# Optimization experiments

Measured on AMD Instinct MI355X. Metric: run time of the kernel, lower is better.

The kernel has to match this reference:

```python
import jax, jax.numpy as jnp
import numpy as np

N = 100000   # num_nodes
E = 300000   # num directed edges (symmetrized to 2E inside forward)
D = 128      # input_dim
O = 128      # output_dim
R = 32       # num_relations
B = 8        # num_bases


def setup_inputs() -> dict:
    key = jax.random.key(0)
    ks = jax.random.split(key, 8)
    x = jax.random.normal(ks[0], (N, D), dtype=jnp.float32)
    node_keep_mask = jax.random.randint(ks[1], (N,), 0, 2) > 0
    source = jax.random.randint(ks[2], (E,), 0, N, dtype=jnp.int32)
    target = jax.random.randint(ks[3], (E,), 0, N, dtype=jnp.int32)
    edge_type = jax.random.randint(ks[4], (E,), 0, R, dtype=jnp.int32)
    edge_weights = jax.random.uniform(ks[5], (E,), dtype=jnp.float32)
    # xavier_normal for bases
    std = (2.0 / (D + O)) ** 0.5
    bases = jax.random.normal(ks[6], (B, D, O), dtype=jnp.float32) * std
    # uniform then L1-normalized rows, shape (R+1, B); row R is the self-loop
    rbw = jax.random.uniform(ks[7], (R + 1, B), dtype=jnp.float32)
    rbw = rbw / jnp.sum(rbw, axis=1, keepdims=True)
    return {
        "x": x,
        "node_keep_mask": node_keep_mask,
        "source": source,
        "target": target,
        "edge_type": edge_type,
        "edge_weights": edge_weights,
        "bases": bases,
        "relation_base_weights": rbw,
    }


def reference(x, node_keep_mask, source, target, edge_type, edge_weights,
              bases, relation_base_weights):
    # Self-loop: weight for relation id == num_relations (last row)
    w_self = jnp.einsum("bij,b->ij", bases, relation_base_weights[-1])
    out = jnp.where(node_keep_mask[:, None], x @ w_self, jnp.zeros((), x.dtype))

    # Symmetrize edges: messages flow in both directions (same relation/weight)
    src = jnp.concatenate([source, target])          # (2E,)
    tgt = jnp.concatenate([target, source])          # (2E,)
    etype = jnp.concatenate([edge_type, edge_type])  # (2E,)
    ew = jnp.concatenate([edge_weights, edge_weights])  # (2E,)

    # Project all nodes through every basis once: (N, B, O)
    proj = jnp.einsum("nd,bdo->nbo", x, bases)
    # Per-edge basis coefficients from the edge's relation: (2E, B)
    coeff = relation_base_weights[etype]
    # Message: x[src] @ (sum_b coeff_b * base_b) == sum_b coeff_b * proj[src, b]
    msg = jnp.einsum("eb,ebo->eo", coeff, proj[src])  # (2E, O)
    msg = msg * ew[:, None]

    # Scatter-add messages into target nodes
    out = out.at[tgt].add(msg)
    return out
```

## Files before the change

### kernel.cpp

```cpp
#include <hip/hip_runtime.h>

typedef __attribute__((ext_vector_type(8))) __bf16 bf16x8;
typedef __attribute__((ext_vector_type(4))) float f32x4;
typedef __attribute__((ext_vector_type(8))) unsigned short ushortx8;

__device__ inline unsigned short f2bf(float f) {
  unsigned int u = __float_as_uint(f);
  unsigned int r = (u + 0x7FFFu + ((u >> 16) & 1u)) >> 16;
  return (unsigned short)r;
}

__global__ __launch_bounds__(256) void conv_kernel(const float* __restrict__ x,
                                                   unsigned short* __restrict__ xb,
                                                   int total8) {
  int id = blockIdx.x * 256 + threadIdx.x;
  if (id >= total8) return;
  f32x4 f0 = ((const f32x4*)x)[2 * id];
  f32x4 f1 = ((const f32x4*)x)[2 * id + 1];
  ushortx8 r;
  r[0] = f2bf(f0[0]); r[1] = f2bf(f0[1]); r[2] = f2bf(f0[2]); r[3] = f2bf(f0[3]);
  r[4] = f2bf(f1[0]); r[5] = f2bf(f1[1]); r[6] = f2bf(f1[2]); r[7] = f2bf(f1[3]);
  ((ushortx8*)xb)[id] = r;
}

__global__ __launch_bounds__(256) void tconv_kernel(const float* __restrict__ bases,
                                                    unsigned short* __restrict__ bmt) {
  int id = blockIdx.x * 256 + threadIdx.x;
  if (id >= 128 * 1024) return;
  int o = id >> 10, k = id & 1023, b = k >> 7, d = k & 127;
  bmt[id] = f2bf(bases[b * 16384 + d * 128 + o]);
}

__global__ void detect_kernel(const unsigned char* __restrict__ mask, int nbytes,
                              int* __restrict__ flag_out) {
  __shared__ int nz_off, big;
  if (threadIdx.x == 0) { nz_off = 0; big = 0; }
  __syncthreads();
  int lnz = 0, lbig = 0;
  for (int i = threadIdx.x; i < nbytes; i += 256) {
    unsigned char v = mask[i];
    if ((i & 3) && v) lnz++;
    if (v > 1) lbig++;
  }
  if (lnz) atomicAdd(&nz_off, lnz);
  if (lbig) atomicAdd(&big, lbig);
  __syncthreads();
  if (threadIdx.x == 0) *flag_out = (nz_off == 0) ? 0 : ((big == 0) ? 1 : 2);
}

__global__ __launch_bounds__(256) void hist_kernel(const int* __restrict__ src,
                                                   const int* __restrict__ tgt, int E,
                                                   int* __restrict__ cnt) {
  int i = blockIdx.x * 256 + threadIdx.x;
  if (i >= E) return;
  atomicAdd(&cnt[tgt[i]], 1);
  atomicAdd(&cnt[src[i]], 1);
}

__global__ __launch_bounds__(256) void scan1_kernel(const int* __restrict__ cnt, int N,
                                                    int* __restrict__ bsum) {
  __shared__ int s[256];
  int t = threadIdx.x, i = blockIdx.x * 256 + t;
  s[t] = (i < N) ? cnt[i] : 0;
  __syncthreads();
#pragma unroll
  for (int off = 128; off > 0; off >>= 1) {
    if (t < off) s[t] += s[t + off];
    __syncthreads();
  }
  if (t == 0) bsum[blockIdx.x] = s[0];
}

__global__ void scan2_kernel(const int* __restrict__ bsum, int nb,
                             int* __restrict__ bexcl, int* __restrict__ base, int N) {
  __shared__ int s[512];
  int t = threadIdx.x;
  int v = (t < nb) ? bsum[t] : 0;
  s[t] = v;
  __syncthreads();
  for (int off = 1; off < 512; off <<= 1) {
    int x = (t >= off) ? s[t - off] : 0;
    __syncthreads();
    s[t] += x;
    __syncthreads();
  }
  if (t < nb) bexcl[t] = s[t] - v;
  if (t == nb - 1) base[N] = s[t];
}

__global__ __launch_bounds__(256) void scan3_kernel(const int* __restrict__ cnt, int N,
                                                    const int* __restrict__ bexcl,
                                                    int* __restrict__ base,
                                                    int* __restrict__ cursor) {
  __shared__ int s[256];
  int t = threadIdx.x, i = blockIdx.x * 256 + t;
  int c = (i < N) ? cnt[i] : 0;
  s[t] = c;
  __syncthreads();
  for (int off = 1; off < 256; off <<= 1) {
    int x = (t >= off) ? s[t - off] : 0;
    __syncthreads();
    s[t] += x;
    __syncthreads();
  }
  if (i < N) {
    int v = bexcl[blockIdx.x] + s[t] - c;
    base[i] = v;
    cursor[i] = v;
  }
}

__global__ __launch_bounds__(256) void scatter_kernel(const int* __restrict__ src,
                                                      const int* __restrict__ tgt,
                                                      const int* __restrict__ et,
                                                      const float* __restrict__ ew, int E,
                                                      int* __restrict__ cursor,
                                                      uint2* __restrict__ msrw) {
  int i = blockIdx.x * 256 + threadIdx.x;
  if (i >= E) return;
  int s = src[i], g = tgt[i], r = et[i];
  unsigned wbits = __float_as_uint(ew[i]);
  int s1 = atomicAdd(&cursor[g], 1);
  msrw[s1] = make_uint2((unsigned)s | ((unsigned)r << 24), wbits);
  int s2 = atomicAdd(&cursor[s], 1);
  msrw[s2] = make_uint2((unsigned)g | ((unsigned)r << 24), wbits);
}

__global__ __launch_bounds__(512, 4) void gather_kernel(
    const unsigned* __restrict__ xb32, const unsigned short* __restrict__ bmt,
    const int* __restrict__ base, const uint2* __restrict__ msrw,
    const float* __restrict__ rbw, const void* __restrict__ maskp,
    const int* __restrict__ flag_p, float* __restrict__ out, int N) {
  extern __shared__ char smem[];
  float* ctab = (float*)(smem + 65536);
  int t = threadIdx.x;
  for (int i = t; i < 264; i += 512) ctab[i] = rbw[i];
  int wid = t >> 6, l = t & 63;
  int t0 = blockIdx.x * 32;
  int flag = *flag_p;
  __syncthreads();

#pragma unroll
  for (int pr = 0; pr < 2; ++pr) {
    int tgA = t0 + wid * 4 + pr * 2;
    int tgc[2], beg[2], cnt[2];
    float zlo[2][8], zhi[2][8];
    uint2 srw0[2], srw1[2];
    unsigned x0[2];
#pragma unroll
    for (int p = 0; p < 2; ++p) {
      int tg = tgA + p;
      tgc[p] = (tg < N) ? tg : (N - 1);
    }
    int b0 = base[tgc[0]], b1 = base[tgc[0] + 1], b2 = base[tgc[1] + 1];
    beg[0] = b0; cnt[0] = (tgA < N) ? (b1 - b0) : 0;
    beg[1] = base[tgc[1]];
    cnt[1] = (tgA + 1 < N) ? (b2 - beg[1]) : 0;
#pragma unroll
    for (int p = 0; p < 2; ++p) {
      int tg = tgA + p;
      unsigned xs = xb32[(size_t)tgc[p] * 64 + l];
      bool keep;
      if (flag == 0)      keep = ((const int*)maskp)[tgc[p]] != 0;
      else if (flag == 1) keep = ((const unsigned char*)maskp)[tgc[p]] != 0;
      else                keep = ((const float*)maskp)[tgc[p]] != 0.f;
      float ms = (keep && tg < N) ? 1.f : 0.f;
      float slo = __uint_as_float(xs << 16);
      float shi = __uint_as_float(xs & 0xFFFF0000u);
#pragma unroll
      for (int b = 0; b < 8; ++b) {
        float a = ms * ctab[256 + b];
        zlo[p][b] = a * slo;
        zhi[p][b] = a * shi;
      }
      srw0[p] = make_uint2(0u, 0u);
      srw1[p] = make_uint2(0u, 0u);
      x0[p] = 0u;
      if (cnt[p] > 0) srw0[p] = msrw[beg[p]];
      if (cnt[p] > 1) srw1[p] = msrw[beg[p] + 1];
      if (cnt[p] > 0) x0[p] = xb32[(size_t)(srw0[p].x & 0xFFFFFFu) * 64 + l];
    }
    int mmax = max(cnt[0], cnt[1]);
    for (int m = 0; m < mmax; ++m) {
#pragma unroll
      for (int p = 0; p < 2; ++p) {
        if (m < cnt[p]) {
          int i2 = (m + 2 < cnt[p]) ? (beg[p] + m + 2) : beg[p];
          uint2 srw2 = msrw[i2];
          unsigned x1 = xb32[(size_t)(srw1[p].x & 0xFFFFFFu) * 64 + l];
          int rel = srw0[p].x >> 24;
          float w = __uint_as_float(srw0[p].y);
          f32x4 c0 = *(const f32x4*)&ctab[rel * 8];
          f32x4 c1 = *(const f32x4*)&ctab[rel * 8 + 4];
          float cc[8] = {c0[0], c0[1], c0[2], c0[3], c1[0], c1[1], c1[2], c1[3]};
          float lo = __uint_as_float(x0[p] << 16);
          float hi = __uint_as_float(x0[p] & 0xFFFF0000u);
#pragma unroll
          for (int b = 0; b < 8; ++b) {
            float a = w * cc[b];
            zlo[p][b] = fmaf(a, lo, zlo[p][b]);
            zhi[p][b] = fmaf(a, hi, zhi[p][b]);
          }
          srw0[p] = srw1[p]; x0[p] = x1; srw1[p] = srw2;
        }
      }
    }
#pragma unroll
    for (int p = 0; p < 2; ++p) {
      int row = wid * 4 + pr * 2 + p;
#pragma unroll
      for (int b = 0; b < 8; ++b) {
        unsigned pk = (unsigned)f2bf(zlo[p][b]) | ((unsigned)f2bf(zhi[p][b]) << 16);
        int byte = row * 2048 + ((b * 256 + l * 4) ^ ((row & 7) << 4));
        *(unsigned*)(smem + byte) = pk;
      }
    }
  }
  __syncthreads();

  int l15 = l & 15, lk8 = (l >> 4) * 8;
  f32x4 acc[2] = {};
  for (int ks = 0; ks < 32; ++ks) {
    int k0 = ks * 32 + lk8;
    bf16x8 a[2], bb;
#pragma unroll
    for (int rt = 0; rt < 2; ++rt) {
      int tr = rt * 16 + l15;
      int byte = tr * 2048 + ((k0 * 2) ^ ((tr & 7) << 4));
      a[rt] = *(const bf16x8*)(smem + byte);
    }
    int col = wid * 16 + l15;
    bb = *(const bf16x8*)(bmt + (size_t)col * 1024 + k0);
#pragma unroll
    for (int rt = 0; rt < 2; ++rt)
      acc[rt] = __builtin_amdgcn_mfma_f32_16x16x32_bf16(a[rt], bb, acc[rt], 0, 0, 0);
  }
#pragma unroll
  for (int rt = 0; rt < 2; ++rt) {
    int rowb = t0 + rt * 16 + (l >> 4) * 4;
    int col = wid * 16 + l15;
#pragma unroll
    for (int i = 0; i < 4; ++i) {
      int row = rowb + i;
      if (row < N) out[(size_t)row * 128 + col] = acc[rt][i];
    }
  }
}

extern "C" void kernel_launch(void* const* d_in, const int* in_sizes, int n_in,
                              void* d_out, int out_size, void* d_ws, size_t ws_size,
                              hipStream_t stream) {
  const float* x = (const float*)d_in[0];
  const void* mask = d_in[1];
  const int* source = (const int*)d_in[2];
  const int* target = (const int*)d_in[3];
  const int* etype = (const int*)d_in[4];
  const float* eweight = (const float*)d_in[5];
  const float* bases = (const float*)d_in[6];
  const float* rbw = (const float*)d_in[7];
  float* out = (float*)d_out;

  const int N = in_sizes[1];
  const int E = in_sizes[2];
  const int M = 2 * E;
  const int NB = (N + 255) / 256;

  char* ws = (char*)d_ws;
  size_t off = 0;
  unsigned short* xb = (unsigned short*)(ws + off); off += (size_t)N * 256;
  unsigned short* bmt = (unsigned short*)(ws + off); off += 128 * 1024 * 2;
  uint2* msrw = (uint2*)(ws + off); off += (size_t)(M + 4) * 8;
  int* base = (int*)(ws + off); off += ((size_t)N + 64) * 4;
  int* cursor = (int*)(ws + off); off += ((size_t)N + 64) * 4;
  int* cnt = (int*)(ws + off); off += ((size_t)N + 64) * 4;
  int* bsum = (int*)(ws + off); off += 2048;
  int* bexcl = (int*)(ws + off); off += 2048;
  int* flag = (int*)(ws + off); off += 256;

  hipMemsetAsync(cnt, 0, (size_t)N * 4, stream);
  detect_kernel<<<1, 256, 0, stream>>>((const unsigned char*)mask, N < 8192 ? N : 8192, flag);
  int total8 = (N * 128) / 8;
  conv_kernel<<<(total8 + 255) / 256, 256, 0, stream>>>(x, xb, total8);
  tconv_kernel<<<(128 * 1024 + 255) / 256, 256, 0, stream>>>(bases, bmt);
  hist_kernel<<<(E + 255) / 256, 256, 0, stream>>>(source, target, E, cnt);
  scan1_kernel<<<NB, 256, 0, stream>>>(cnt, N, bsum);
  scan2_kernel<<<1, 512, 0, stream>>>(bsum, NB, bexcl, base, N);
  scan3_kernel<<<NB, 256, 0, stream>>>(cnt, N, bexcl, base, cursor);
  scatter_kernel<<<(E + 255) / 256, 256, 0, stream>>>(source, target, etype, eweight, E,
                                                      cursor, msrw);
  int gblk = (N + 31) / 32;
  size_t shmem = 65536 + 264 * sizeof(float) + 16;
  gather_kernel<<<gblk, 512, shmem, stream>>>((const unsigned*)xb, bmt, base, msrw,
                                              rbw, mask, flag, out, N);
}
```

Baseline: 283.0 us.

## Fuse prep kernels and batch edge-metadata loads per warp with shuffles

Merges the bf16 conversion of x, the transposed conversion of bases and the mask-format detection into one launch using block-range dispatch, removing two kernel launches. In the gather kernel, each warp now handles its four target nodes one after another. It loads up to 64 edge records at once (one per lane), broadcasts them with shuffles, and issues eight independent x-row gathers before doing the FMAs. This replaces the serial two-deep prefetch chain, which aims to expose more memory-level parallelism, at the cost of extra shuffles and more register pressure.

Measured after the change: 279.9 us. About the same (-1.1%).

```diff
diff --git a/kernel.cpp b/kernel.cpp
--- a/kernel.cpp
+++ b/kernel.cpp
@@ -10,42 +10,43 @@
   return (unsigned short)r;
 }
 
-__global__ __launch_bounds__(256) void conv_kernel(const float* __restrict__ x,
-                                                   unsigned short* __restrict__ xb,
-                                                   int total8) {
-  int id = blockIdx.x * 256 + threadIdx.x;
-  if (id >= total8) return;
-  f32x4 f0 = ((const f32x4*)x)[2 * id];
-  f32x4 f1 = ((const f32x4*)x)[2 * id + 1];
-  ushortx8 r;
-  r[0] = f2bf(f0[0]); r[1] = f2bf(f0[1]); r[2] = f2bf(f0[2]); r[3] = f2bf(f0[3]);
-  r[4] = f2bf(f1[0]); r[5] = f2bf(f1[1]); r[6] = f2bf(f1[2]); r[7] = f2bf(f1[3]);
-  ((ushortx8*)xb)[id] = r;
-}
-
-__global__ __launch_bounds__(256) void tconv_kernel(const float* __restrict__ bases,
-                                                    unsigned short* __restrict__ bmt) {
-  int id = blockIdx.x * 256 + threadIdx.x;
-  if (id >= 128 * 1024) return;
-  int o = id >> 10, k = id & 1023, b = k >> 7, d = k & 127;
-  bmt[id] = f2bf(bases[b * 16384 + d * 128 + o]);
-}
-
-__global__ void detect_kernel(const unsigned char* __restrict__ mask, int nbytes,
-                              int* __restrict__ flag_out) {
-  __shared__ int nz_off, big;
-  if (threadIdx.x == 0) { nz_off = 0; big = 0; }
-  __syncthreads();
-  int lnz = 0, lbig = 0;
-  for (int i = threadIdx.x; i < nbytes; i += 256) {
-    unsigned char v = mask[i];
-    if ((i & 3) && v) lnz++;
-    if (v > 1) lbig++;
-  }
-  if (lnz) atomicAdd(&nz_off, lnz);
-  if (lbig) atomicAdd(&big, lbig);
-  __syncthreads();
-  if (threadIdx.x == 0) *flag_out = (nz_off == 0) ? 0 : ((big == 0) ? 1 : 2);
+__global__ __launch_bounds__(256) void prep_kernel(const float* __restrict__ x,
+                                                   unsigned short* __restrict__ xb, int total8,
+                                                   const float* __restrict__ bases,
+                                                   unsigned short* __restrict__ bmt,
+                                                   const unsigned char* __restrict__ mask,
+                                                   int mbytes, int* __restrict__ flag_out,
+                                                   int CB, int TB) {
+  int bid = blockIdx.x;
+  if (bid < CB) {
+    int id = bid * 256 + threadIdx.x;
+    if (id >= total8) return;
+    f32x4 f0 = ((const f32x4*)x)[2 * id];
+    f32x4 f1 = ((const f32x4*)x)[2 * id + 1];
+    ushortx8 r;
+    r[0] = f2bf(f0[0]); r[1] = f2bf(f0[1]); r[2] = f2bf(f0[2]); r[3] = f2bf(f0[3]);
+    r[4] = f2bf(f1[0]); r[5] = f2bf(f1[1]); r[6] = f2bf(f1[2]); r[7] = f2bf(f1[3]);
+    ((ushortx8*)xb)[id] = r;
+  } else if (bid < CB + TB) {
+    int id = (bid - CB) * 256 + threadIdx.x;
+    if (id >= 128 * 1024) return;
+    int o = id >> 10, k = id & 1023, b = k >> 7, d = k & 127;
+    bmt[id] = f2bf(bases[b * 16384 + d * 128 + o]);
+  } else {
+    __shared__ int nz_off, big;
+    if (threadIdx.x == 0) { nz_off = 0; big = 0; }
+    __syncthreads();
+    int lnz = 0, lbig = 0;
+    for (int i = threadIdx.x; i < mbytes; i += 256) {
+      unsigned char v = mask[i];
+      if ((i & 3) && v) lnz++;
+      if (v > 1) lbig++;
+    }
+    if (lnz) atomicAdd(&nz_off, lnz);
+    if (lbig) atomicAdd(&big, lbig);
+    __syncthreads();
+    if (threadIdx.x == 0) *flag_out = (nz_off == 0) ? 0 : ((big == 0) ? 1 : 2);
+  }
 }
 
 __global__ __launch_bounds__(256) void hist_kernel(const int* __restrict__ src,
@@ -140,80 +141,95 @@
   int flag = *flag_p;
   __syncthreads();
 
-#pragma unroll
-  for (int pr = 0; pr < 2; ++pr) {
-    int tgA = t0 + wid * 4 + pr * 2;
-    int tgc[2], beg[2], cnt[2];
-    float zlo[2][8], zhi[2][8];
-    uint2 srw0[2], srw1[2];
-    unsigned x0[2];
-#pragma unroll
-    for (int p = 0; p < 2; ++p) {
-      int tg = tgA + p;
-      tgc[p] = (tg < N) ? tg : (N - 1);
-    }
-    int b0 = base[tgc[0]], b1 = base[tgc[0] + 1], b2 = base[tgc[1] + 1];
-    beg[0] = b0; cnt[0] = (tgA < N) ? (b1 - b0) : 0;
-    beg[1] = base[tgc[1]];
-    cnt[1] = (tgA + 1 < N) ? (b2 - beg[1]) : 0;
-#pragma unroll
-    for (int p = 0; p < 2; ++p) {
-      int tg = tgA + p;
-      unsigned xs = xb32[(size_t)tgc[p] * 64 + l];
-      bool keep;
-      if (flag == 0)      keep = ((const int*)maskp)[tgc[p]] != 0;
-      else if (flag == 1) keep = ((const unsigned char*)maskp)[tgc[p]] != 0;
-      else                keep = ((const float*)maskp)[tgc[p]] != 0.f;
-      float ms = (keep && tg < N) ? 1.f : 0.f;
-      float slo = __uint_as_float(xs << 16);
-      float shi = __uint_as_float(xs & 0xFFFF0000u);
+  int tgbase = t0 + wid * 4;
+  int bv = 0;
+  if (l < 5) bv = base[min(tgbase + (int)l, N)];
+  int baseArr[5];
+#pragma unroll
+  for (int j = 0; j < 5; ++j) baseArr[j] = __shfl(bv, j);
+
+  unsigned xself[4];
+  float msk[4];
+#pragma unroll
+  for (int j = 0; j < 4; ++j) {
+    int tg = tgbase + j;
+    int tgc = min(tg, N - 1);
+    xself[j] = xb32[(size_t)tgc * 64 + l];
+    bool keep;
+    if (flag == 0)      keep = ((const int*)maskp)[tgc] != 0;
+    else if (flag == 1) keep = ((const unsigned char*)maskp)[tgc] != 0;
+    else                keep = ((const float*)maskp)[tgc] != 0.f;
+    msk[j] = (keep && tg < N) ? 1.f : 0.f;
+  }
+
+  uint2 srwl = make_uint2(0u, 0u);
+  {
+    int c = (tgbase < N) ? (baseArr[1] - baseArr[0]) : 0;
+    if (c > 0) srwl = msrw[baseArr[0] + min((int)l, c - 1)];
+  }
+
+  for (int j = 0; j < 4; ++j) {
+    int tg = tgbase + j;
+    int beg = baseArr[j];
+    int cnt = (tg < N) ? (baseArr[j + 1] - beg) : 0;
+    float zlo[8], zhi[8];
+    {
+      float slo = __uint_as_float(xself[j] << 16);
+      float shi = __uint_as_float(xself[j] & 0xFFFF0000u);
 #pragma unroll
       for (int b = 0; b < 8; ++b) {
-        float a = ms * ctab[256 + b];
-        zlo[p][b] = a * slo;
-        zhi[p][b] = a * shi;
+        float a = msk[j] * ctab[256 + b];
+        zlo[b] = a * slo;
+        zhi[b] = a * shi;
       }
-      srw0[p] = make_uint2(0u, 0u);
-      srw1[p] = make_uint2(0u, 0u);
-      x0[p] = 0u;
-      if (cnt[p] > 0) srw0[p] = msrw[beg[p]];
-      if (cnt[p] > 1) srw1[p] = msrw[beg[p] + 1];
-      if (cnt[p] > 0) x0[p] = xb32[(size_t)(srw0[p].x & 0xFFFFFFu) * 64 + l];
-    }
-    int mmax = max(cnt[0], cnt[1]);
-    for (int m = 0; m < mmax; ++m) {
-#pragma unroll
-      for (int p = 0; p < 2; ++p) {
-        if (m < cnt[p]) {
-          int i2 = (m + 2 < cnt[p]) ? (beg[p] + m + 2) : beg[p];
-          uint2 srw2 = msrw[i2];
-          unsigned x1 = xb32[(size_t)(srw1[p].x & 0xFFFFFFu) * 64 + l];
-          int rel = srw0[p].x >> 24;
-          float w = __uint_as_float(srw0[p].y);
-          f32x4 c0 = *(const f32x4*)&ctab[rel * 8];
-          f32x4 c1 = *(const f32x4*)&ctab[rel * 8 + 4];
-          float cc[8] = {c0[0], c0[1], c0[2], c0[3], c1[0], c1[1], c1[2], c1[3]};
-          float lo = __uint_as_float(x0[p] << 16);
-          float hi = __uint_as_float(x0[p] & 0xFFFF0000u);
+    }
+    uint2 cur = srwl;
+    if (j < 3) {
+      int cn = (tg + 1 < N) ? (baseArr[j + 2] - baseArr[j + 1]) : 0;
+      srwl = make_uint2(0u, 0u);
+      if (cn > 0) srwl = msrw[baseArr[j + 1] + min((int)l, cn - 1)];
+    }
+    for (int mb = 0; mb < cnt; mb += 64) {
+      if (mb > 0) cur = msrw[beg + mb + min((int)l, cnt - mb - 1)];
+      int blk = min(cnt - mb, 64);
+      for (int c0 = 0; c0 < blk; c0 += 8) {
+        unsigned sx[8], xr[8];
+        float wv[8];
+#pragma unroll
+        for (int s = 0; s < 8; ++s) {
+          int m = c0 + s;
+          int msel = (m < blk) ? m : 0;
+          unsigned a = __shfl(cur.x, msel);
+          unsigned wb = __shfl(cur.y, msel);
+          sx[s] = a;
+          wv[s] = (m < blk) ? __uint_as_float(wb) : 0.f;
+          unsigned row = (m < blk) ? (a & 0xFFFFFFu) : 0u;
+          xr[s] = xb32[(size_t)row * 64 + l];
+        }
+#pragma unroll
+        for (int s = 0; s < 8; ++s) {
+          int rel = (int)(sx[s] >> 24);
+          f32x4 cA = *(const f32x4*)&ctab[rel * 8];
+          f32x4 cB = *(const f32x4*)&ctab[rel * 8 + 4];
+          float cc[8] = {cA[0], cA[1], cA[2], cA[3], cB[0], cB[1], cB[2], cB[3]};
+          float lo = __uint_as_float(xr[s] << 16);
+          float hi = __uint_as_float(xr[s] & 0xFFFF0000u);
+          float w = wv[s];
 #pragma unroll
           for (int b = 0; b < 8; ++b) {
             float a = w * cc[b];
-            zlo[p][b] = fmaf(a, lo, zlo[p][b]);
-            zhi[p][b] = fmaf(a, hi, zhi[p][b]);
+            zlo[b] = fmaf(a, lo, zlo[b]);
+            zhi[b] = fmaf(a, hi, zhi[b]);
           }
-          srw0[p] = srw1[p]; x0[p] = x1; srw1[p] = srw2;
         }
       }
     }
-#pragma unroll
-    for (int p = 0; p < 2; ++p) {
-      int row = wid * 4 + pr * 2 + p;
-#pragma unroll
-      for (int b = 0; b < 8; ++b) {
-        unsigned pk = (unsigned)f2bf(zlo[p][b]) | ((unsigned)f2bf(zhi[p][b]) << 16);
-        int byte = row * 2048 + ((b * 256 + l * 4) ^ ((row & 7) << 4));
-        *(unsigned*)(smem + byte) = pk;
-      }
+    int row = wid * 4 + j;
+#pragma unroll
+    for (int b = 0; b < 8; ++b) {
+      unsigned pk = (unsigned)f2bf(zlo[b]) | ((unsigned)f2bf(zhi[b]) << 16);
+      int byte = row * 2048 + ((b * 256 + l * 4) ^ ((row & 7) << 4));
+      *(unsigned*)(smem + byte) = pk;
     }
   }
   __syncthreads();
@@ -278,10 +294,12 @@
   int* flag = (int*)(ws + off); off += 256;
 
   hipMemsetAsync(cnt, 0, (size_t)N * 4, stream);
-  detect_kernel<<<1, 256, 0, stream>>>((const unsigned char*)mask, N < 8192 ? N : 8192, flag);
   int total8 = (N * 128) / 8;
-  conv_kernel<<<(total8 + 255) / 256, 256, 0, stream>>>(x, xb, total8);
-  tconv_kernel<<<(128 * 1024 + 255) / 256, 256, 0, stream>>>(bases, bmt);
+  int CB = (total8 + 255) / 256;
+  int TB = (128 * 1024 + 255) / 256;
+  prep_kernel<<<CB + TB + 1, 256, 0, stream>>>(x, xb, total8, bases, bmt,
+                                               (const unsigned char*)mask,
+                                               N < 8192 ? N : 8192, flag, CB, TB);
   hist_kernel<<<(E + 255) / 256, 256, 0, stream>>>(source, target, E, cnt);
   scan1_kernel<<<NB, 256, 0, stream>>>(cnt, N, bsum);
   scan2_kernel<<<1, 512, 0, stream>>>(bsum, NB, bexcl, base, N);
```
